# Optimization experiments

Measured on AMD Instinct MI355X. Metric: run time of the kernel, lower is better.

The kernel has to match this reference:

```python
import jax, jax.numpy as jnp
import numpy as np

KERNEL_SIZE = (8,)

def setup_inputs() -> dict:
    key = jax.random.key(0)
    k1, = jax.random.split(key, 1)
    inputs = jax.random.normal(k1, (32, 131072, 8), dtype=jnp.float32)
    w = jnp.ones(KERNEL_SIZE, dtype=jnp.float32)  # initializer='ones', non-trainable
    return {"inputs": inputs, "w": w}

def reference(inputs, w):
    # keys[b, n] = sum_c inputs[b, n, c] * w[c]
    keys = jnp.einsum('bnc,c->bn', inputs, w)
    idx = jnp.argsort(keys, axis=-1)                     # [B, N] int
    # batched gather: out[b, i, :] = inputs[b, idx[b, i], :]
    out = jnp.take_along_axis(inputs, idx[:, :, None], axis=1)
    return out
```

## Files before the change

### kernel.cpp

```cpp
#include <hip/hip_runtime.h>


#define NB   32
#define NPB  131072
#define NK   (NB * NPB)
#define TPB  256
#define EPT  16
#define EPB  (TPB * EPT)
#define BPB  (NPB / EPB)
#define NBLK (NB * BPB)
#define BINS 256

typedef unsigned long long u64;
typedef unsigned int u32;

__device__ __forceinline__ u32 fkey(float x) {
    u32 u = __float_as_uint(x);
    return u ^ ((u & 0x80000000u) ? 0xFFFFFFFFu : 0x80000000u);
}

__device__ __forceinline__ u64 matchany(u32 d) {
    u64 m = ~0ull;
    #pragma unroll
    for (int k = 0; k < 8; ++k) {
        u64 bk = __ballot((d >> k) & 1u);
        m &= ((d >> k) & 1u) ? bk : ~bk;
    }
    return m;
}

__global__ void khist0(const float* __restrict__ in, const float* __restrict__ w,
                       u64* __restrict__ outp, u32* __restrict__ hist)
{
    __shared__ u32 h[BINS];
    int t = threadIdx.x;
    h[t] = 0;
    __syncthreads();
    int b = blockIdx.x / BPB, blk = blockIdx.x % BPB;
    size_t base = (size_t)b * NPB + (size_t)blk * EPB;
    int lane = t & 63;
    float w0 = w[0], w1 = w[1], w2 = w[2], w3 = w[3];
    float w4 = w[4], w5 = w[5], w6 = w[6], w7 = w[7];
    #pragma unroll
    for (int i = 0; i < EPT; ++i) {
        size_t row = base + t + i * TPB;
        const float4* p = (const float4*)in + row * 2;
        float4 a = p[0], c = p[1];
        float k = __fmul_rn(a.x, w0);
        k = __fadd_rn(k, __fmul_rn(a.y, w1));
        k = __fadd_rn(k, __fmul_rn(a.z, w2));
        k = __fadd_rn(k, __fmul_rn(a.w, w3));
        k = __fadd_rn(k, __fmul_rn(c.x, w4));
        k = __fadd_rn(k, __fmul_rn(c.y, w5));
        k = __fadd_rn(k, __fmul_rn(c.z, w6));
        k = __fadd_rn(k, __fmul_rn(c.w, w7));
        u32 fk = fkey(k);
        outp[row] = ((u64)fk << 32) | (u64)((u32)row & (NPB - 1));
        u32 d = fk & 255u;
        u64 m = matchany(d);
        if (lane == __ffsll(m) - 1) atomicAdd(&h[d], (u32)__popcll(m));
    }
    __syncthreads();
    hist[(b * BINS + t) * BPB + blk] = h[t];
}

__global__ void rhist(const u64* __restrict__ src, u32* __restrict__ hist, int shift)
{
    __shared__ u32 h[BINS];
    int t = threadIdx.x;
    h[t] = 0;
    __syncthreads();
    int b = blockIdx.x / BPB, blk = blockIdx.x % BPB;
    size_t base = (size_t)b * NPB + (size_t)blk * EPB;
    int lane = t & 63;
    #pragma unroll
    for (int i = 0; i < EPT; ++i) {
        u64 v = src[base + t + i * TPB];
        u32 d = (u32)(v >> shift) & 255u;
        u64 m = matchany(d);
        if (lane == __ffsll(m) - 1) atomicAdd(&h[d], (u32)__popcll(m));
    }
    __syncthreads();
    hist[(b * BINS + t) * BPB + blk] = h[t];
}

__global__ void rscan(u32* __restrict__ hist)
{
    int b = blockIdx.x, t = threadIdx.x;
    u32* H = hist + b * BINS * BPB;
    u32 v[32], s = 0;
    #pragma unroll
    for (int k = 0; k < 32; ++k) { v[k] = H[t * 32 + k]; s += v[k]; }
    int lane = t & 63, wid = t >> 6;
    u32 inc = s;
    #pragma unroll
    for (int off = 1; off < 64; off <<= 1) {
        u32 y = __shfl_up(inc, off, 64);
        if (lane >= off) inc += y;
    }
    __shared__ u32 wsum[4];
    if (lane == 63) wsum[wid] = inc;
    __syncthreads();
    u32 wo = 0;
    #pragma unroll
    for (int wI = 0; wI < 4; ++wI) if (wI < wid) wo += wsum[wI];
    u32 run = wo + inc - s;
    #pragma unroll
    for (int k = 0; k < 32; ++k) { u32 c = v[k]; H[t * 32 + k] = run; run += c; }
}

#define RANK_PERMUTE_BODY(SRC_EXPR)                                             \
    int t = threadIdx.x, lane = t & 63, wid = t >> 6;                           \
    size_t base = (size_t)b * NPB + (size_t)blk * EPB + (size_t)wid * 1024;     \
    _Pragma("unroll")                                                           \
    for (int k = 0; k < 4; ++k) ((u32*)s_wcnt)[t + k * TPB] = 0;                \
    __syncthreads();                                                            \
    u64 v[EPT];                                                                 \
    u32 rnk[EPT];                                                               \
    _Pragma("unroll")                                                           \
    for (int i = 0; i < EPT; ++i) v[i] = (SRC_EXPR);                            \
    _Pragma("unroll")                                                           \
    for (int i = 0; i < EPT; ++i) {                                             \
        u32 d = (u32)(v[i] >> shift) & 255u;                                    \
        u64 m = matchany(d);                                                    \
        int leader = __ffsll(m) - 1;                                            \
        u32 baseCnt = 0;                                                        \
        if (lane == leader) {                                                   \
            baseCnt = s_wcnt[wid][d];                                           \
            s_wcnt[wid][d] = baseCnt + (u32)__popcll(m);                        \
        }                                                                       \
        baseCnt = __shfl(baseCnt, leader, 64);                                  \
        rnk[i] = baseCnt + (u32)__popcll(m & ((1ull << lane) - 1ull));          \
        __builtin_amdgcn_wave_barrier();                                        \
    }                                                                           \
    __syncthreads();                                                            \
    u32 c0 = s_wcnt[0][t], c1 = s_wcnt[1][t], c2 = s_wcnt[2][t], c3 = s_wcnt[3][t]; \
    u32 tot = c0 + c1 + c2 + c3;                                                \
    s_wcnt[0][t] = 0; s_wcnt[1][t] = c0; s_wcnt[2][t] = c0 + c1;                \
    s_wcnt[3][t] = c0 + c1 + c2;                                                \
    u32 inc = tot;                                                              \
    _Pragma("unroll")                                                           \
    for (int off = 1; off < 64; off <<= 1) {                                    \
        u32 y = __shfl_up(inc, off, 64);                                        \
        if (lane >= off) inc += y;                                              \
    }                                                                           \
    if (lane == 63) s_wsum[wid] = inc;                                          \
    __syncthreads();                                                            \
    u32 wo = 0;                                                                 \
    _Pragma("unroll")                                                           \
    for (int wI = 0; wI < 4; ++wI) if (wI < wid) wo += s_wsum[wI];              \
    s_dbase[t] = wo + inc - tot;                                                \
    s_gbase[t] = hist[(b * BINS + t) * BPB + blk];                              \
    __syncthreads();                                                            \
    _Pragma("unroll")                                                           \
    for (int i = 0; i < EPT; ++i) {                                             \
        u32 d = (u32)(v[i] >> shift) & 255u;                                    \
        u32 pos = s_dbase[d] + s_wcnt[wid][d] + rnk[i];                         \
        s_key[pos] = (u32)(v[i] >> 32);                                         \
        s_idx[pos] = (u32)v[i];                                                 \
    }                                                                           \
    __syncthreads();

__launch_bounds__(TPB, 4)
__global__ void rscatter(const u64* __restrict__ src, u64* __restrict__ dst,
                         const u32* __restrict__ hist, int shift)
{
    __shared__ u32 s_key[EPB];
    __shared__ u32 s_idx[EPB];
    __shared__ u32 s_wcnt[4][BINS];
    __shared__ u32 s_dbase[BINS];
    __shared__ u32 s_gbase[BINS];
    __shared__ u32 s_wsum[4];
    int b = blockIdx.x / BPB, blk = blockIdx.x % BPB;
    RANK_PERMUTE_BODY(src[base + i * 64 + lane])

    int kshift = shift - 32;
    #pragma unroll
    for (int i = 0; i < EPT; ++i) {
        int j = i * TPB + t;
        u32 key = s_key[j], idx = s_idx[j];
        u32 d = (key >> kshift) & 255u;
        u32 gpos = s_gbase[d] + (u32)j - s_dbase[d];
        dst[(size_t)b * NPB + gpos] = ((u64)key << 32) | (u64)idx;
    }
}

__launch_bounds__(TPB, 4)
__global__ void rscatgat(const u64* __restrict__ src, const float* __restrict__ in,
                         float* __restrict__ out, const u32* __restrict__ hist)
{
    __shared__ u32 s_key[EPB];
    __shared__ u32 s_idx[EPB];
    __shared__ u32 s_wcnt[4][BINS];
    __shared__ u32 s_dbase[BINS];
    __shared__ u32 s_gbase[BINS];
    __shared__ u32 s_wsum[4];
    const int shift = 56;
    int i0 = blockIdx.x;
    int xcd = i0 & 7, j0 = i0 >> 3;
    int b = xcd + 8 * (j0 >> 5), blk = j0 & 31;
    RANK_PERMUTE_BODY(src[base + i * 64 + lane])

    const float4* inb = (const float4*)in + ((size_t)b << 18);
    float4* outb = (float4*)out + ((size_t)b << 18);
    #pragma unroll
    for (int i = 0; i < EPT; ++i) {
        int j = i * TPB + t;
        u32 key = s_key[j], idx = s_idx[j];
        u32 d = (key >> 24);
        u32 gpos = s_gbase[d] + (u32)j - s_dbase[d];
        const float4* s = inb + (size_t)idx * 2;
        float4 x = s[0], y = s[1];
        float4* drow = outb + (size_t)gpos * 2;
        drow[0] = x; drow[1] = y;
    }
}

extern "C" void kernel_launch(void* const* d_in, const int* in_sizes, int n_in,
                              void* d_out, int out_size, void* d_ws, size_t ws_size,
                              hipStream_t stream)
{
    const float* in = (const float*)d_in[0];
    const float* w  = (const float*)d_in[1];
    float* out = (float*)d_out;

    u64* A = (u64*)d_ws;
    u64* B = (u64*)d_out;
    u32* hist = (u32*)((char*)d_ws + (size_t)NK * 8);

    khist0<<<NBLK, TPB, 0, stream>>>(in, w, B, hist);
    rscan<<<NB, TPB, 0, stream>>>(hist);
    rscatter<<<NBLK, TPB, 0, stream>>>(B, A, hist, 32);

    rhist<<<NBLK, TPB, 0, stream>>>(A, hist, 40);
    rscan<<<NB, TPB, 0, stream>>>(hist);
    rscatter<<<NBLK, TPB, 0, stream>>>(A, B, hist, 40);

    rhist<<<NBLK, TPB, 0, stream>>>(B, hist, 48);
    rscan<<<NB, TPB, 0, stream>>>(hist);
    rscatter<<<NBLK, TPB, 0, stream>>>(B, A, hist, 48);

    rhist<<<NBLK, TPB, 0, stream>>>(A, hist, 56);
    rscan<<<NB, TPB, 0, stream>>>(hist);
    rscatgat<<<NBLK, TPB, 0, stream>>>(A, in, out, hist);
}
```

Before: 222.8 us.

## Compress final radix pass to 32-bit packed digit+index entries

```diff
diff --git a/kernel.cpp b/kernel.cpp
--- a/kernel.cpp
+++ b/kernel.cpp
@@ -77,6 +77,26 @@
     for (int i = 0; i < EPT; ++i) {
         u64 v = src[base + t + i * TPB];
         u32 d = (u32)(v >> shift) & 255u;
+        u64 m = matchany(d);
+        if (lane == __ffsll(m) - 1) atomicAdd(&h[d], (u32)__popcll(m));
+    }
+    __syncthreads();
+    hist[(b * BINS + t) * BPB + blk] = h[t];
+}
+
+__global__ void rhist32(const u32* __restrict__ src, u32* __restrict__ hist)
+{
+    __shared__ u32 h[BINS];
+    int t = threadIdx.x;
+    h[t] = 0;
+    __syncthreads();
+    int b = blockIdx.x / BPB, blk = blockIdx.x % BPB;
+    size_t base = (size_t)b * NPB + (size_t)blk * EPB;
+    int lane = t & 63;
+    #pragma unroll
+    for (int i = 0; i < EPT; ++i) {
+        u32 v = src[base + t + i * TPB];
+        u32 d = v >> 24;
         u64 m = matchany(d);
         if (lane == __ffsll(m) - 1) atomicAdd(&h[d], (u32)__popcll(m));
     }
@@ -186,8 +206,8 @@
 }
 
 __launch_bounds__(TPB, 4)
-__global__ void rscatgat(const u64* __restrict__ src, const float* __restrict__ in,
-                         float* __restrict__ out, const u32* __restrict__ hist)
+__global__ void rscat2c(const u64* __restrict__ src, u32* __restrict__ dstc,
+                        const u32* __restrict__ hist)
 {
     __shared__ u32 s_key[EPB];
     __shared__ u32 s_idx[EPB];
@@ -195,19 +215,94 @@
     __shared__ u32 s_dbase[BINS];
     __shared__ u32 s_gbase[BINS];
     __shared__ u32 s_wsum[4];
-    const int shift = 56;
+    const int shift = 48;
+    int b = blockIdx.x / BPB, blk = blockIdx.x % BPB;
+    RANK_PERMUTE_BODY(src[base + i * 64 + lane])
+
+    #pragma unroll
+    for (int i = 0; i < EPT; ++i) {
+        int j = i * TPB + t;
+        u32 key = s_key[j], idx = s_idx[j];
+        u32 d = (key >> 16) & 255u;
+        u32 gpos = s_gbase[d] + (u32)j - s_dbase[d];
+        dstc[(size_t)b * NPB + gpos] = (key & 0xFF000000u) | idx;
+    }
+}
+
+__launch_bounds__(TPB, 6)
+__global__ void rscatgat32(const u32* __restrict__ src, const float* __restrict__ in,
+                           float* __restrict__ out, const u32* __restrict__ hist)
+{
+    __shared__ u32 s_pack[EPB];
+    __shared__ u32 s_wcnt[4][BINS];
+    __shared__ u32 s_dbase[BINS];
+    __shared__ u32 s_gbase[BINS];
+    __shared__ u32 s_wsum[4];
     int i0 = blockIdx.x;
     int xcd = i0 & 7, j0 = i0 >> 3;
     int b = xcd + 8 * (j0 >> 5), blk = j0 & 31;
-    RANK_PERMUTE_BODY(src[base + i * 64 + lane])
+
+    int t = threadIdx.x, lane = t & 63, wid = t >> 6;
+    size_t base = (size_t)b * NPB + (size_t)blk * EPB + (size_t)wid * 1024;
+    #pragma unroll
+    for (int k = 0; k < 4; ++k) ((u32*)s_wcnt)[t + k * TPB] = 0;
+    __syncthreads();
+
+    u32 v[EPT];
+    u32 rnk[EPT];
+    #pragma unroll
+    for (int i = 0; i < EPT; ++i) v[i] = src[base + i * 64 + lane];
+
+    #pragma unroll
+    for (int i = 0; i < EPT; ++i) {
+        u32 d = v[i] >> 24;
+        u64 m = matchany(d);
+        int leader = __ffsll(m) - 1;
+        u32 baseCnt = 0;
+        if (lane == leader) {
+            baseCnt = s_wcnt[wid][d];
+            s_wcnt[wid][d] = baseCnt + (u32)__popcll(m);
+        }
+        baseCnt = __shfl(baseCnt, leader, 64);
+        rnk[i] = baseCnt + (u32)__popcll(m & ((1ull << lane) - 1ull));
+        __builtin_amdgcn_wave_barrier();
+    }
+    __syncthreads();
+
+    u32 c0 = s_wcnt[0][t], c1 = s_wcnt[1][t], c2 = s_wcnt[2][t], c3 = s_wcnt[3][t];
+    u32 tot = c0 + c1 + c2 + c3;
+    s_wcnt[0][t] = 0; s_wcnt[1][t] = c0; s_wcnt[2][t] = c0 + c1; s_wcnt[3][t] = c0 + c1 + c2;
+    u32 inc = tot;
+    #pragma unroll
+    for (int off = 1; off < 64; off <<= 1) {
+        u32 y = __shfl_up(inc, off, 64);
+        if (lane >= off) inc += y;
+    }
+    if (lane == 63) s_wsum[wid] = inc;
+    __syncthreads();
+    u32 wo = 0;
+    #pragma unroll
+    for (int wI = 0; wI < 4; ++wI) if (wI < wid) wo += s_wsum[wI];
+    s_dbase[t] = wo + inc - tot;
+    s_gbase[t] = hist[(b * BINS + t) * BPB + blk];
+    __syncthreads();
+
+    #pragma unroll
+    for (int i = 0; i < EPT; ++i) {
+        u32 d = v[i] >> 24;
+        u32 pos = s_dbase[d] + s_wcnt[wid][d] + rnk[i];
+        s_pack[pos] = v[i];
+    }
+    __syncthreads();
 
     const float4* inb = (const float4*)in + ((size_t)b << 18);
     float4* outb = (float4*)out + ((size_t)b << 18);
     #pragma unroll
     for (int i = 0; i < EPT; ++i) {
         int j = i * TPB + t;
-        u32 key = s_key[j], idx = s_idx[j];
-        u32 d = (key >> 24);
+        u32 pack = s_pack[j];
+        u32 d = pack >> 24;
+        u32 idx = pack & 0x1FFFFu;
         u32 gpos = s_gbase[d] + (u32)j - s_dbase[d];
         const float4* s = inb + (size_t)idx * 2;
         float4 x = s[0], y = s[1];
@@ -224,8 +319,9 @@
     const float* w  = (const float*)d_in[1];
     float* out = (float*)d_out;
 
-    u64* A = (u64*)d_ws;
-    u64* B = (u64*)d_out;
+    u64* A   = (u64*)d_ws;
+    u32* A32 = (u32*)d_ws;
+    u64* B   = (u64*)d_out;
     u32* hist = (u32*)((char*)d_ws + (size_t)NK * 8);
 
     khist0<<<NBLK, TPB, 0, stream>>>(in, w, B, hist);
@@ -238,9 +334,9 @@
 
     rhist<<<NBLK, TPB, 0, stream>>>(B, hist, 48);
     rscan<<<NB, TPB, 0, stream>>>(hist);
-    rscatter<<<NBLK, TPB, 0, stream>>>(B, A, hist, 48);
-
-    rhist<<<NBLK, TPB, 0, stream>>>(A, hist, 56);
+    rscat2c<<<NBLK, TPB, 0, stream>>>(B, A32, hist);
+
+    rhist32<<<NBLK, TPB, 0, stream>>>(A32, hist);
     rscan<<<NB, TPB, 0, stream>>>(hist);
-    rscatgat<<<NBLK, TPB, 0, stream>>>(A, in, out, hist);
-}
+    rscatgat32<<<NBLK, TPB, 0, stream>>>(A32, in, out, hist);
+}
```

Result: slower. 234.1 us (+5.1%).
